# Performance work log

Hardware: AMD Instinct MI355X
Metric: run time of the kernel (lower is better)

## Reference

```python
import jax, jax.numpy as jnp
import numpy as np

B = 16384          # batch size
NNZ_PER = 32       # active features per board (max pieces)
FT_OUT = 1024
BUCKETS = 8
FEAT = 768


def setup_inputs() -> dict:
    key = jax.random.key(0)
    k1, k2, k3, k4, k5, k6, k7 = jax.random.split(key, 7)
    nnz = B * NNZ_PER
    b_idx = jnp.repeat(jnp.arange(B, dtype=jnp.int64), NNZ_PER)
    stm_f = jax.random.randint(k1, (nnz,), 0, FEAT, dtype=jnp.int64)
    nstm_f = jax.random.randint(k2, (nnz,), 0, FEAT, dtype=jnp.int64)
    stm_indices = jnp.stack([b_idx, stm_f], axis=1)
    nstm_indices = jnp.stack([b_idx, nstm_f], axis=1)
    values = jnp.ones((nnz,), dtype=jnp.float32)
    buckets = jax.random.randint(k3, (B,), 0, BUCKETS, dtype=jnp.int64)
    ft_w = jax.random.normal(k4, (FT_OUT, FEAT), dtype=jnp.float32) * 0.02
    ft_b = jax.random.normal(k5, (FT_OUT,), dtype=jnp.float32) * 0.02
    out_w = jax.random.normal(k6, (BUCKETS, 2 * FT_OUT), dtype=jnp.float32) * 0.02
    out_b = jax.random.normal(k7, (BUCKETS,), dtype=jnp.float32) * 0.02
    return {"stm_indices": stm_indices, "nstm_indices": nstm_indices,
            "values": values, "buckets": buckets, "size": B,
            "ft_w": ft_w, "ft_b": ft_b, "out_w": out_w, "out_b": out_b}


def _to_dense(indices, values, size):
    # sparse_coo_tensor(...).to_dense(): duplicate coords sum
    board = jnp.zeros((size, FEAT), dtype=values.dtype)
    return board.at[indices[:, 0], indices[:, 1]].add(values)


def reference(stm_indices, nstm_indices, values, buckets, size, ft_w, ft_b, out_w, out_b):
    board_stm = _to_dense(stm_indices, values, size)    # [B, 768]
    board_nstm = _to_dense(nstm_indices, values, size)  # [B, 768]
    stm_ft = board_stm @ ft_w.T + ft_b                  # [B, FT_OUT]
    nstm_ft = board_nstm @ ft_w.T + ft_b
    hidden = jnp.clip(jnp.concatenate([stm_ft, nstm_ft], axis=1), 0.0, 1.0)  # [B, 2*FT_OUT]
    l1 = hidden @ out_w.T + out_b                       # [B, BUCKETS]
    # per-row bucket gather == view(-1,1)[buckets + arange(B)*bucket_count]
    l1_out = jnp.take_along_axis(l1, buckets[:, None], axis=1)  # [B, 1]
    return jax.nn.sigmoid(l1_out)
```

## Files before the change

kernel.cpp:

```cpp
#include <hip/hip_runtime.h>
#include <hip/hip_bf16.h>
#include <math.h>

#define B_SZ    16384
#define NNZ     32
#define FT_OUT  1024
#define FEAT    768
#define BUCKETS 8

typedef __attribute__((ext_vector_type(8))) short short8;

__device__ __forceinline__ float b2f(unsigned short u) {
    union { unsigned int i; float f; } x;
    x.i = ((unsigned int)u) << 16;
    return x.f;
}

__global__ __launch_bounds__(256) void transpose_ftw_bf16(
    const float* __restrict__ ft_w, unsigned short* __restrict__ ftT) {
    __shared__ float tile[32][33];
    const int fo = blockIdx.x * 32;
    const int oo = blockIdx.y * 32;
    const int tx = threadIdx.x & 31;
    const int ty = threadIdx.x >> 5;
#pragma unroll
    for (int i = 0; i < 4; ++i)
        tile[ty + 8 * i][tx] = ft_w[(oo + ty + 8 * i) * FEAT + fo + tx];
    __syncthreads();
#pragma unroll
    for (int i = 0; i < 4; ++i) {
        float v = tile[tx][ty + 8 * i];
        ftT[(fo + ty + 8 * i) * FT_OUT + oo + tx] =
            (unsigned short)(__bfloat16_as_ushort(__float2bfloat16(v)));
    }
}

__global__ __launch_bounds__(256) void nn_fwd(
    const int*            __restrict__ stm_idx,
    const int*            __restrict__ nstm_idx,
    const float*          __restrict__ values,
    const int*            __restrict__ buckets,
    const unsigned short* __restrict__ ftT,
    const float*          __restrict__ ft_b,
    const float*          __restrict__ out_w,
    const float*          __restrict__ out_b,
    float*                __restrict__ out)
{
    const int wave = threadIdx.x >> 6;
    const int lane = threadIdx.x & 63;
    const int b = __builtin_amdgcn_readfirstlane(blockIdx.x * 4 + wave);

    float acc_s[2][8], acc_n[2][8];
#pragma unroll
    for (int c = 0; c < 2; ++c) {
        const float4* fb = (const float4*)(ft_b + c * 512 + lane * 8);
        float4 b0 = fb[0], b1 = fb[1];
        acc_s[c][0] = b0.x; acc_s[c][1] = b0.y; acc_s[c][2] = b0.z; acc_s[c][3] = b0.w;
        acc_s[c][4] = b1.x; acc_s[c][5] = b1.y; acc_s[c][6] = b1.z; acc_s[c][7] = b1.w;
#pragma unroll
        for (int j = 0; j < 8; ++j) acc_n[c][j] = acc_s[c][j];
    }

    const int base = b * NNZ;

#pragma unroll 4
    for (int k = 0; k < NNZ; ++k) {
        const int   fs = stm_idx [(base + k) * 2 + 1];
        const int   fn = nstm_idx[(base + k) * 2 + 1];
        const float v  = values[base + k];
        const unsigned short* cs = ftT + fs * FT_OUT;
        const unsigned short* cn = ftT + fn * FT_OUT;
#pragma unroll
        for (int c = 0; c < 2; ++c) {
            short8 ws = *(const short8*)(cs + c * 512 + lane * 8);
            short8 wn = *(const short8*)(cn + c * 512 + lane * 8);
#pragma unroll
            for (int j = 0; j < 8; ++j) {
                acc_s[c][j] = fmaf(v, b2f((unsigned short)ws[j]), acc_s[c][j]);
                acc_n[c][j] = fmaf(v, b2f((unsigned short)wn[j]), acc_n[c][j]);
            }
        }
    }

    const int bkt = __builtin_amdgcn_readfirstlane(buckets[b]);
    const float* ow = out_w + bkt * (2 * FT_OUT);

    float part = 0.0f;
#pragma unroll
    for (int c = 0; c < 2; ++c) {
        const float4* ps = (const float4*)(ow + c * 512 + lane * 8);
        const float4* pn = (const float4*)(ow + FT_OUT + c * 512 + lane * 8);
        float4 s0 = ps[0], s1 = ps[1], n0 = pn[0], n1 = pn[1];
        const float* wsp = &s0.x;
        part += fminf(fmaxf(acc_s[c][0], 0.f), 1.f) * s0.x;
        part += fminf(fmaxf(acc_s[c][1], 0.f), 1.f) * s0.y;
        part += fminf(fmaxf(acc_s[c][2], 0.f), 1.f) * s0.z;
        part += fminf(fmaxf(acc_s[c][3], 0.f), 1.f) * s0.w;
        part += fminf(fmaxf(acc_s[c][4], 0.f), 1.f) * s1.x;
        part += fminf(fmaxf(acc_s[c][5], 0.f), 1.f) * s1.y;
        part += fminf(fmaxf(acc_s[c][6], 0.f), 1.f) * s1.z;
        part += fminf(fmaxf(acc_s[c][7], 0.f), 1.f) * s1.w;
        part += fminf(fmaxf(acc_n[c][0], 0.f), 1.f) * n0.x;
        part += fminf(fmaxf(acc_n[c][1], 0.f), 1.f) * n0.y;
        part += fminf(fmaxf(acc_n[c][2], 0.f), 1.f) * n0.z;
        part += fminf(fmaxf(acc_n[c][3], 0.f), 1.f) * n0.w;
        part += fminf(fmaxf(acc_n[c][4], 0.f), 1.f) * n1.x;
        part += fminf(fmaxf(acc_n[c][5], 0.f), 1.f) * n1.y;
        part += fminf(fmaxf(acc_n[c][6], 0.f), 1.f) * n1.z;
        part += fminf(fmaxf(acc_n[c][7], 0.f), 1.f) * n1.w;
        (void)wsp;
    }
#pragma unroll
    for (int off = 32; off >= 1; off >>= 1)
        part += __shfl_xor(part, off);

    if (lane == 0) {
        float logit = part + out_b[bkt];
        out[b] = 1.0f / (1.0f + expf(-logit));
    }
}

extern "C" void kernel_launch(void* const* d_in, const int* in_sizes, int n_in,
                              void* d_out, int out_size, void* d_ws, size_t ws_size,
                              hipStream_t stream) {
    const int*   stm_idx  = (const int*)  d_in[0];
    const int*   nstm_idx = (const int*)  d_in[1];
    const float* values   = (const float*)d_in[2];
    const int*   buckets  = (const int*)  d_in[3];
    const float* ft_w     = (const float*)d_in[5];
    const float* ft_b     = (const float*)d_in[6];
    const float* out_w    = (const float*)d_in[7];
    const float* out_b    = (const float*)d_in[8];
    float*       out      = (float*)d_out;

    unsigned short* ftT = (unsigned short*)d_ws;

    transpose_ftw_bf16<<<dim3(FEAT / 32, FT_OUT / 32), 256, 0, stream>>>(ft_w, ftT);

    nn_fwd<<<B_SZ / 4, 256, 0, stream>>>(stm_idx, nstm_idx, values, buckets,
                                         ftT, ft_b, out_w, out_b, out);
}
```

Measured before the change: 152.3 us.

## Densify boards and compute feature transformer via bf16 MFMA GEMM with fused head

Replaces the per-board sparse row-gather accumulation with a pipeline. It materializes dense bf16 boards for both sides, runs a tiled bf16 MFMA GEMM against the bf16 weights, and fuses the bias, clamp and bucket-selected output dot product into the epilogue with atomic accumulation into per-board logits. A final kernel applies the output bias and sigmoid. This trades a large amount of redundant gather traffic for dense tensor-core work, plus extra memory traffic for the dense boards and atomics. The old path is kept as a fallback when the workspace is too small.

```diff
diff --git a/kernel.cpp b/kernel.cpp
--- a/kernel.cpp
+++ b/kernel.cpp
@@ -7,117 +7,219 @@
 #define FT_OUT  1024
 #define FEAT    768
 #define BUCKETS 8
-
+#define M_TOT   (2 * B_SZ)
+
+typedef __bf16 bf16x8 __attribute__((ext_vector_type(8)));
+typedef float  f32x4  __attribute__((ext_vector_type(4)));
 typedef __attribute__((ext_vector_type(8))) short short8;
 
+__device__ __forceinline__ unsigned short f2b(float f) {
+    return __bfloat16_as_ushort(__float2bfloat16(f));
+}
 __device__ __forceinline__ float b2f(unsigned short u) {
-    union { unsigned int i; float f; } x;
-    x.i = ((unsigned int)u) << 16;
-    return x.f;
+    union { unsigned int i; float f; } x; x.i = ((unsigned int)u) << 16; return x.f;
+}
+__device__ __forceinline__ void gld_lds16(const void* g, void* l) {
+    __builtin_amdgcn_global_load_lds(
+        (const __attribute__((address_space(1))) unsigned int*)g,
+        (__attribute__((address_space(3))) unsigned int*)l, 16, 0, 0);
+}
+
+__global__ __launch_bounds__(256) void build_boards(
+    const int*   __restrict__ stm_idx, const int* __restrict__ nstm_idx,
+    const float* __restrict__ values,  unsigned short* __restrict__ A) {
+    __shared__ float rowbuf[4][FEAT];
+    const int wave = threadIdx.x >> 6, lane = threadIdx.x & 63;
+    const int m = blockIdx.x * 4 + wave;
+    const int board = m & (B_SZ - 1);
+    const int* idx = (m >= B_SZ) ? nstm_idx : stm_idx;
+    float* rb = rowbuf[wave];
+#pragma unroll
+    for (int i = 0; i < FEAT / 64; ++i) rb[i * 64 + lane] = 0.0f;
+    __syncthreads();
+    if (lane < NNZ) {
+        int   f = idx[(board * NNZ + lane) * 2 + 1];
+        float v = values[board * NNZ + lane];
+        atomicAdd(&rb[f], v);
+    }
+    __syncthreads();
+    unsigned int* dst = (unsigned int*)(A + (long)m * FEAT);
+#pragma unroll
+    for (int i = 0; i < FEAT / 128; ++i) {
+        int e = i * 64 + lane;
+        unsigned int lo = f2b(rb[2 * e]), hi = f2b(rb[2 * e + 1]);
+        dst[e] = lo | (hi << 16);
+    }
+}
+
+__global__ __launch_bounds__(256) void cvt_ftw(const float2* __restrict__ src,
+                                               unsigned int* __restrict__ dst) {
+    int i = blockIdx.x * 256 + threadIdx.x;
+    float2 v = src[i];
+    dst[i] = (unsigned int)f2b(v.x) | ((unsigned int)f2b(v.y) << 16);
+}
+
+#define BM 128
+#define BN 128
+#define BK 64
+
+__global__ __launch_bounds__(256) void gemm_head(
+    const unsigned short* __restrict__ A,
+    const unsigned short* __restrict__ W,
+    const float* __restrict__ ft_b,
+    const float* __restrict__ out_w,
+    const int*   __restrict__ buckets,
+    float*       __restrict__ logit)
+{
+    __shared__ unsigned short smA[BM * BK];
+    __shared__ unsigned short smB[BN * BK];
+    const int wave = threadIdx.x >> 6, lane = threadIdx.x & 63;
+    const int wm = wave >> 1, wn = wave & 1;
+    const int tileM = blockIdx.x * BM;
+    const int tileN = blockIdx.y * BN;
+
+    f32x4 acc[4][4] = {};
+
+    const int srow = wave * 32 + (lane >> 3);
+    const int skoff = (lane & 7) * 8;
+
+    for (int kt = 0; kt < FEAT / BK; ++kt) {
+        const int k0 = kt * BK;
+        __syncthreads();
+#pragma unroll
+        for (int q = 0; q < 4; ++q) {
+            int r = srow + q * 8;
+            gld_lds16(A + (long)(tileM + r) * FEAT + k0 + skoff, smA + (wave * 32 + q * 8) * BK);
+            gld_lds16(W + (long)(tileN + r) * FEAT + k0 + skoff, smB + (wave * 32 + q * 8) * BK);
+        }
+        __syncthreads();
+#pragma unroll
+        for (int ki = 0; ki < 2; ++ki) {
+            bf16x8 af[4], bfr[4];
+#pragma unroll
+            for (int f = 0; f < 4; ++f) {
+                af[f]  = *(const bf16x8*)(smA + (wm * 64 + f * 16 + (lane & 15)) * BK + ki * 32 + (lane >> 4) * 8);
+                bfr[f] = *(const bf16x8*)(smB + (wn * 64 + f * 16 + (lane & 15)) * BK + ki * 32 + (lane >> 4) * 8);
+            }
+#pragma unroll
+            for (int mf = 0; mf < 4; ++mf)
+#pragma unroll
+                for (int nf = 0; nf < 4; ++nf)
+                    acc[mf][nf] = __builtin_amdgcn_mfma_f32_16x16x32_bf16(
+                        af[mf], bfr[nf], acc[mf][nf], 0, 0, 0);
+        }
+    }
+
+    float ftb[4]; int cols[4];
+#pragma unroll
+    for (int nf = 0; nf < 4; ++nf) {
+        cols[nf] = tileN + wn * 64 + nf * 16 + (lane & 15);
+        ftb[nf]  = ft_b[cols[nf]];
+    }
+    const int sideoff = (tileM >= B_SZ) ? FT_OUT : 0;
+
+#pragma unroll
+    for (int mf = 0; mf < 4; ++mf) {
+#pragma unroll
+        for (int r = 0; r < 4; ++r) {
+            int mloc  = wm * 64 + mf * 16 + (lane >> 4) * 4 + r;
+            int board = (tileM + mloc) & (B_SZ - 1);
+            int bkt   = buckets[board];
+            const float* ow = out_w + bkt * (2 * FT_OUT) + sideoff;
+            float p = 0.0f;
+#pragma unroll
+            for (int nf = 0; nf < 4; ++nf) {
+                float h = acc[mf][nf][r] + ftb[nf];
+                h = fminf(fmaxf(h, 0.0f), 1.0f);
+                p += h * ow[cols[nf]];
+            }
+            p += __shfl_xor(p, 1);
+            p += __shfl_xor(p, 2);
+            p += __shfl_xor(p, 4);
+            p += __shfl_xor(p, 8);
+            if ((lane & 15) == 0) atomicAdd(logit + board, p);
+        }
+    }
+}
+
+__global__ __launch_bounds__(256) void finish(const float* __restrict__ logit,
+                                              const int* __restrict__ buckets,
+                                              const float* __restrict__ out_b,
+                                              float* __restrict__ out) {
+    int b = blockIdx.x * 256 + threadIdx.x;
+    float l = logit[b] + out_b[buckets[b]];
+    out[b] = 1.0f / (1.0f + expf(-l));
 }
 
 __global__ __launch_bounds__(256) void transpose_ftw_bf16(
     const float* __restrict__ ft_w, unsigned short* __restrict__ ftT) {
     __shared__ float tile[32][33];
-    const int fo = blockIdx.x * 32;
-    const int oo = blockIdx.y * 32;
-    const int tx = threadIdx.x & 31;
-    const int ty = threadIdx.x >> 5;
+    const int fo = blockIdx.x * 32, oo = blockIdx.y * 32;
+    const int tx = threadIdx.x & 31, ty = threadIdx.x >> 5;
 #pragma unroll
     for (int i = 0; i < 4; ++i)
         tile[ty + 8 * i][tx] = ft_w[(oo + ty + 8 * i) * FEAT + fo + tx];
     __syncthreads();
 #pragma unroll
-    for (int i = 0; i < 4; ++i) {
-        float v = tile[tx][ty + 8 * i];
-        ftT[(fo + ty + 8 * i) * FT_OUT + oo + tx] =
-            (unsigned short)(__bfloat16_as_ushort(__float2bfloat16(v)));
-    }
+    for (int i = 0; i < 4; ++i)
+        ftT[(fo + ty + 8 * i) * FT_OUT + oo + tx] = f2b(tile[tx][ty + 8 * i]);
 }
 
 __global__ __launch_bounds__(256) void nn_fwd(
-    const int*            __restrict__ stm_idx,
-    const int*            __restrict__ nstm_idx,
-    const float*          __restrict__ values,
-    const int*            __restrict__ buckets,
-    const unsigned short* __restrict__ ftT,
-    const float*          __restrict__ ft_b,
-    const float*          __restrict__ out_w,
-    const float*          __restrict__ out_b,
-    float*                __restrict__ out)
-{
-    const int wave = threadIdx.x >> 6;
-    const int lane = threadIdx.x & 63;
+    const int* __restrict__ stm_idx, const int* __restrict__ nstm_idx,
+    const float* __restrict__ values, const int* __restrict__ buckets,
+    const unsigned short* __restrict__ ftT, const float* __restrict__ ft_b,
+    const float* __restrict__ out_w, const float* __restrict__ out_b,
+    float* __restrict__ out) {
+    const int wave = threadIdx.x >> 6, lane = threadIdx.x & 63;
     const int b = __builtin_amdgcn_readfirstlane(blockIdx.x * 4 + wave);
-
     float acc_s[2][8], acc_n[2][8];
 #pragma unroll
     for (int c = 0; c < 2; ++c) {
         const float4* fb = (const float4*)(ft_b + c * 512 + lane * 8);
         float4 b0 = fb[0], b1 = fb[1];
-        acc_s[c][0] = b0.x; acc_s[c][1] = b0.y; acc_s[c][2] = b0.z; acc_s[c][3] = b0.w;
-        acc_s[c][4] = b1.x; acc_s[c][5] = b1.y; acc_s[c][6] = b1.z; acc_s[c][7] = b1.w;
-#pragma unroll
-        for (int j = 0; j < 8; ++j) acc_n[c][j] = acc_s[c][j];
-    }
-
+        float t[8] = {b0.x,b0.y,b0.z,b0.w,b1.x,b1.y,b1.z,b1.w};
+#pragma unroll
+        for (int j = 0; j < 8; ++j) { acc_s[c][j] = t[j]; acc_n[c][j] = t[j]; }
+    }
     const int base = b * NNZ;
-
 #pragma unroll 4
     for (int k = 0; k < NNZ; ++k) {
-        const int   fs = stm_idx [(base + k) * 2 + 1];
-        const int   fn = nstm_idx[(base + k) * 2 + 1];
-        const float v  = values[base + k];
+        const int fs = stm_idx[(base + k) * 2 + 1];
+        const int fn = nstm_idx[(base + k) * 2 + 1];
+        const float v = values[base + k];
         const unsigned short* cs = ftT + fs * FT_OUT;
         const unsigned short* cn = ftT + fn * FT_OUT;
 #pragma unroll
         for (int c = 0; c < 2; ++c) {
             short8 ws = *(const short8*)(cs + c * 512 + lane * 8);
-            short8 wn = *(const short8*)(cn + c * 512 + lane * 8);
+            short8 wn2 = *(const short8*)(cn + c * 512 + lane * 8);
 #pragma unroll
             for (int j = 0; j < 8; ++j) {
                 acc_s[c][j] = fmaf(v, b2f((unsigned short)ws[j]), acc_s[c][j]);
-                acc_n[c][j] = fmaf(v, b2f((unsigned short)wn[j]), acc_n[c][j]);
+                acc_n[c][j] = fmaf(v, b2f((unsigned short)wn2[j]), acc_n[c][j]);
             }
         }
     }
-
     const int bkt = __builtin_amdgcn_readfirstlane(buckets[b]);
     const float* ow = out_w + bkt * (2 * FT_OUT);
-
     float part = 0.0f;
 #pragma unroll
     for (int c = 0; c < 2; ++c) {
         const float4* ps = (const float4*)(ow + c * 512 + lane * 8);
         const float4* pn = (const float4*)(ow + FT_OUT + c * 512 + lane * 8);
         float4 s0 = ps[0], s1 = ps[1], n0 = pn[0], n1 = pn[1];
-        const float* wsp = &s0.x;
-        part += fminf(fmaxf(acc_s[c][0], 0.f), 1.f) * s0.x;
-        part += fminf(fmaxf(acc_s[c][1], 0.f), 1.f) * s0.y;
-        part += fminf(fmaxf(acc_s[c][2], 0.f), 1.f) * s0.z;
-        part += fminf(fmaxf(acc_s[c][3], 0.f), 1.f) * s0.w;
-        part += fminf(fmaxf(acc_s[c][4], 0.f), 1.f) * s1.x;
-        part += fminf(fmaxf(acc_s[c][5], 0.f), 1.f) * s1.y;
-        part += fminf(fmaxf(acc_s[c][6], 0.f), 1.f) * s1.z;
-        part += fminf(fmaxf(acc_s[c][7], 0.f), 1.f) * s1.w;
-        part += fminf(fmaxf(acc_n[c][0], 0.f), 1.f) * n0.x;
-        part += fminf(fmaxf(acc_n[c][1], 0.f), 1.f) * n0.y;
-        part += fminf(fmaxf(acc_n[c][2], 0.f), 1.f) * n0.z;
-        part += fminf(fmaxf(acc_n[c][3], 0.f), 1.f) * n0.w;
-        part += fminf(fmaxf(acc_n[c][4], 0.f), 1.f) * n1.x;
-        part += fminf(fmaxf(acc_n[c][5], 0.f), 1.f) * n1.y;
-        part += fminf(fmaxf(acc_n[c][6], 0.f), 1.f) * n1.z;
-        part += fminf(fmaxf(acc_n[c][7], 0.f), 1.f) * n1.w;
-        (void)wsp;
-    }
-#pragma unroll
-    for (int off = 32; off >= 1; off >>= 1)
-        part += __shfl_xor(part, off);
-
-    if (lane == 0) {
-        float logit = part + out_b[bkt];
-        out[b] = 1.0f / (1.0f + expf(-logit));
-    }
+        float sw[8] = {s0.x,s0.y,s0.z,s0.w,s1.x,s1.y,s1.z,s1.w};
+        float nw[8] = {n0.x,n0.y,n0.z,n0.w,n1.x,n1.y,n1.z,n1.w};
+#pragma unroll
+        for (int j = 0; j < 8; ++j) {
+            part += fminf(fmaxf(acc_s[c][j], 0.f), 1.f) * sw[j];
+            part += fminf(fmaxf(acc_n[c][j], 0.f), 1.f) * nw[j];
+        }
+    }
+#pragma unroll
+    for (int off = 32; off >= 1; off >>= 1) part += __shfl_xor(part, off);
+    if (lane == 0) out[b] = 1.0f / (1.0f + expf(-(part + out_b[bkt])));
 }
 
 extern "C" void kernel_launch(void* const* d_in, const int* in_sizes, int n_in,
@@ -133,10 +235,26 @@
     const float* out_b    = (const float*)d_in[8];
     float*       out      = (float*)d_out;
 
-    unsigned short* ftT = (unsigned short*)d_ws;
-
-    transpose_ftw_bf16<<<dim3(FEAT / 32, FT_OUT / 32), 256, 0, stream>>>(ft_w, ftT);
-
-    nn_fwd<<<B_SZ / 4, 256, 0, stream>>>(stm_idx, nstm_idx, values, buckets,
-                                         ftT, ft_b, out_w, out_b, out);
-}
+    const size_t szA = (size_t)M_TOT * FEAT * 2;
+    const size_t szW = (size_t)FT_OUT * FEAT * 2;
+    const size_t NEED = szA + szW + (size_t)B_SZ * 4;
+
+    if (ws_size >= NEED) {
+        unsigned short* A  = (unsigned short*)d_ws;
+        unsigned short* W  = (unsigned short*)((char*)d_ws + szA);
+        float*          lg = (float*)((char*)d_ws + szA + szW);
+
+        cvt_ftw<<<(FT_OUT * FEAT / 2) / 256, 256, 0, stream>>>(
+            (const float2*)ft_w, (unsigned int*)W);
+        build_boards<<<M_TOT / 4, 256, 0, stream>>>(stm_idx, nstm_idx, values, A);
+        hipMemsetAsync(lg, 0, (size_t)B_SZ * 4, stream);
+        gemm_head<<<dim3(M_TOT / BM, FT_OUT / BN), 256, 0, stream>>>(
+            A, W, ft_b, out_w, buckets, lg);
+        finish<<<B_SZ / 256, 256, 0, stream>>>(lg, buckets, out_b, out);
+    } else {
+        unsigned short* ftT = (unsigned short*)d_ws;
+        transpose_ftw_bf16<<<dim3(FEAT / 32, FT_OUT / 32), 256, 0, stream>>>(ft_w, ftT);
+        nn_fwd<<<B_SZ / 4, 256, 0, stream>>>(stm_idx, nstm_idx, values, buckets,
+                                             ftT, ft_b, out_w, out_b, out);
+    }
+}
```

Result: slower. 204.8 us (+34.4%).
